# Kernel tuning notes

Measured on AMD Instinct MI355X. Metric: run time of the kernel, lower is better.

The kernel has to match this reference:

```python
import jax, jax.numpy as jnp
import numpy as np

B, C, F, D = 128, 16, 128, 512


def setup_inputs() -> dict:
    key = jax.random.key(0)
    k1, k2 = jax.random.split(key)
    return {
        "c_feats": jax.random.normal(k1, (B, C, D), dtype=jnp.float32),
        "f_feats": jax.random.normal(k2, (B, F, D), dtype=jnp.float32),
    }


def _dtw_path_masks(S):
    """S: [P, c, f] per-pair similarity. Returns [P, c, f] 0/1 max-path masks.

    DP: D[i,j] = max(D[i-1,j], D[i,j-1], D[i-1,j-1]) + S[i-1,j-1], D[0,0]=0,
    borders -inf. Tie-break priority (up, left, diag) matches Python max().
    Row recurrence is vectorized: D[i,j] = Csum[j] + cummax_k<=j(A[k]-Csum[k-1])
    where A[k]=max(D[i-1,k], D[i-1,k-1]) (wavefront-free row-parallel form).
    """
    P_, c, f = S.shape
    NEG = -jnp.inf

    init = jnp.concatenate([jnp.zeros((P_, 1), S.dtype),
                            jnp.full((P_, f), NEG, S.dtype)], axis=1)  # D[0, 0..f]

    def row_step(prev, dt_row):
        # prev: [P, f+1] = D[i-1, 0..f]; dt_row: [P, f] = S[i-1, :]
        A = jnp.maximum(prev[:, 1:], prev[:, :-1])                  # max(D[i-1,j], D[i-1,j-1])
        Ccum = jnp.cumsum(dt_row, axis=1)
        Cm1 = jnp.concatenate([jnp.zeros((P_, 1), dt_row.dtype), Ccum[:, :-1]], axis=1)
        row = Ccum + jax.lax.cummax(A - Cm1, axis=1)                # D[i, 1..f]
        new_prev = jnp.concatenate([jnp.full((P_, 1), NEG, dt_row.dtype), row], axis=1)
        return new_prev, new_prev

    _, rows = jax.lax.scan(row_step, init, jnp.moveaxis(S, 1, 0))   # [c, P, f+1]
    Dm = jnp.moveaxis(jnp.concatenate([init[None], rows], axis=0), 1, 0)  # [P, c+1, f+1]

    # Predecessor choice per cell; argmax picks first max -> priority up,left,diag
    up = Dm[:, :-1, 1:]
    left = Dm[:, 1:, :-1]
    diag = Dm[:, :-1, :-1]
    mv = jnp.argmax(jnp.stack([up, left, diag], axis=-1), axis=-1).astype(jnp.int32)
    mv = jnp.pad(mv, ((0, 0), (1, 0), (1, 0)))                      # [P, c+1, f+1]

    pidx = jnp.arange(P_)

    def bt_step(carry, _):
        mask, i, j = carry
        active = (i > 0) | (j > 0)
        mask = mask.at[pidx, i - 1, j - 1].add(jnp.where(active, 1.0, 0.0).astype(mask.dtype))
        m = mv[pidx, i, j]
        di = jnp.where(m == 1, 0, 1)   # left keeps i
        dj = jnp.where(m == 0, 0, 1)   # up keeps j
        i = jnp.where(active, i - di, i)
        j = jnp.where(active, j - dj, j)
        return (mask, i, j), None

    mask0 = jnp.zeros((P_, c, f), jnp.float32)
    i0 = jnp.full((P_,), c, jnp.int32)
    j0 = jnp.full((P_,), f, jnp.int32)
    (mask, _, _), _ = jax.lax.scan(bt_step, (mask0, i0, j0), None, length=c + f)
    return mask


def reference(c_feats, f_feats):
    b, c, d = c_feats.shape
    f = f_feats.shape[1]
    xn = c_feats / jnp.linalg.norm(c_feats, axis=-1, keepdims=True)
    yn = f_feats / jnp.linalg.norm(f_feats, axis=-1, keepdims=True)
    # Source quirk: y row j is normalized only once outer index i reaches it
    # (y[i-1] bug), so S[i,j] uses normalized y[j] iff j <= i, raw y[j] otherwise.
    Sn = jnp.einsum('mcd,nfd->mncf', xn, yn)
    Sr = jnp.einsum('mcd,nfd->mncf', xn, f_feats)
    tri = jnp.arange(f)[None, :] <= jnp.arange(c)[:, None]          # [c, f]: j <= i
    S = jnp.where(tri, Sn, Sr).reshape(b * b, c, f)
    return _dtw_path_masks(S).reshape(b, b, c, f)
```

## Files before the change

kernel.cpp:

```cpp
#include <hip/hip_runtime.h>
#include <stdint.h>

#define M_TOT 2048
#define N_TOT 16384
#define K_TOT 512

typedef _Float16 f16x8 __attribute__((ext_vector_type(8)));
typedef float f32x4 __attribute__((ext_vector_type(4)));

#define AS1 __attribute__((address_space(1)))
#define AS3 __attribute__((address_space(3)))

__device__ __forceinline__ void ld_lds16(const void* g, void* l) {
    __builtin_amdgcn_global_load_lds((const AS1 void*)g, (AS3 void*)l, 16, 0, 0);
}

__device__ __forceinline__ void split4(float x0, float x1, float x2, float x3,
                                       uint2* hs, uint2* ls) {
    union U { _Float16 h[4]; uint2 u; } H, L;
    _Float16 h0 = (_Float16)x0; H.h[0] = h0; L.h[0] = (_Float16)(x0 - (float)h0);
    _Float16 h1 = (_Float16)x1; H.h[1] = h1; L.h[1] = (_Float16)(x1 - (float)h1);
    _Float16 h2 = (_Float16)x2; H.h[2] = h2; L.h[2] = (_Float16)(x2 - (float)h2);
    _Float16 h3 = (_Float16)x3; H.h[3] = h3; L.h[3] = (_Float16)(x3 - (float)h3);
    *hs = H.u; *ls = L.u;
}

__global__ __launch_bounds__(256) void norm_split_kernel(
    const float* __restrict__ c_feats, const float* __restrict__ f_feats,
    _Float16* __restrict__ Ah, _Float16* __restrict__ Al,
    _Float16* __restrict__ Bh, _Float16* __restrict__ Bl,
    float* __restrict__ normf)
{
    int wave = blockIdx.x * 4 + (threadIdx.x >> 6);
    int lane = threadIdx.x & 63;
    if (wave < 2048) {
        const float* row = c_feats + (size_t)wave * K_TOT;
        float4 v0 = ((const float4*)row)[lane];
        float4 v1 = ((const float4*)row)[lane + 64];
        double ss = (double)v0.x * v0.x + (double)v0.y * v0.y +
                    (double)v0.z * v0.z + (double)v0.w * v0.w +
                    (double)v1.x * v1.x + (double)v1.y * v1.y +
                    (double)v1.z * v1.z + (double)v1.w * v1.w;
        #pragma unroll
        for (int off = 32; off; off >>= 1) ss += __shfl_down(ss, off);
        double tot = __shfl(ss, 0);
        float nrm = sqrtf((float)tot);
        float a0 = v0.x / nrm, a1 = v0.y / nrm, a2 = v0.z / nrm, a3 = v0.w / nrm;
        float b0 = v1.x / nrm, b1 = v1.y / nrm, b2 = v1.z / nrm, b3 = v1.w / nrm;
        uint2 h, l;
        split4(a0, a1, a2, a3, &h, &l);
        ((uint2*)(Ah + (size_t)wave * K_TOT))[lane] = h;
        ((uint2*)(Al + (size_t)wave * K_TOT))[lane] = l;
        split4(b0, b1, b2, b3, &h, &l);
        ((uint2*)(Ah + (size_t)wave * K_TOT))[lane + 64] = h;
        ((uint2*)(Al + (size_t)wave * K_TOT))[lane + 64] = l;
    } else if (wave < 18432) {
        int fr = wave - 2048;
        const float* row = f_feats + (size_t)fr * K_TOT;
        float4 v0 = ((const float4*)row)[lane];
        float4 v1 = ((const float4*)row)[lane + 64];
        double ss = (double)v0.x * v0.x + (double)v0.y * v0.y +
                    (double)v0.z * v0.z + (double)v0.w * v0.w +
                    (double)v1.x * v1.x + (double)v1.y * v1.y +
                    (double)v1.z * v1.z + (double)v1.w * v1.w;
        #pragma unroll
        for (int off = 32; off; off >>= 1) ss += __shfl_down(ss, off);
        if (lane == 0) normf[fr] = sqrtf((float)ss);
        uint2 h, l;
        split4(v0.x, v0.y, v0.z, v0.w, &h, &l);
        ((uint2*)(Bh + (size_t)fr * K_TOT))[lane] = h;
        ((uint2*)(Bl + (size_t)fr * K_TOT))[lane] = l;
        split4(v1.x, v1.y, v1.z, v1.w, &h, &l);
        ((uint2*)(Bh + (size_t)fr * K_TOT))[lane + 64] = h;
        ((uint2*)(Bl + (size_t)fr * K_TOT))[lane + 64] = l;
    }
}

__global__ __launch_bounds__(256, 2) void mfma_gemm_kernel(
    const _Float16* __restrict__ Ah, const _Float16* __restrict__ Al,
    const _Float16* __restrict__ Bh, const _Float16* __restrict__ Bl,
    const float* __restrict__ normf,
    float* __restrict__ out)
{
    __shared__ _Float16 sAh[128 * 32];
    __shared__ _Float16 sAl[128 * 32];
    __shared__ _Float16 sBh[128 * 32];
    __shared__ _Float16 sBl[128 * 32];

    const int t = threadIdx.x;
    const int w = t >> 6, lane = t & 63;
    const int gm0 = blockIdx.y * 128, gn0 = blockIdx.x * 128;
    const int wm = (w & 1) * 64, wn = (w >> 1) * 64;
    const int fr = lane & 15, fq = lane >> 4;

    f32x4 acc[4][4] = {};

    const int l0 = w * 128 + lane;

    for (int k0 = 0; k0 < K_TOT; k0 += 32) {
        #pragma unroll
        for (int c = 0; c < 2; ++c) {
            int l = l0 + c * 64;
            int row = l >> 2, kq = l & 3;
            size_t goffA = (size_t)(gm0 + row) * K_TOT + k0 + kq * 8;
            size_t goffB = (size_t)(gn0 + row) * K_TOT + k0 + kq * 8;
            ld_lds16(Ah + goffA, sAh + (size_t)l * 8);
            ld_lds16(Al + goffA, sAl + (size_t)l * 8);
            ld_lds16(Bh + goffB, sBh + (size_t)l * 8);
            ld_lds16(Bl + goffB, sBl + (size_t)l * 8);
        }
        __syncthreads();

        f16x8 fah[4], fal[4], fbh[4], fbl[4];
        #pragma unroll
        for (int x = 0; x < 4; ++x) {
            int ar = (wm + x * 16 + fr) * 32 + fq * 8;
            int br = (wn + x * 16 + fr) * 32 + fq * 8;
            fah[x] = *(const f16x8*)(sAh + ar);
            fal[x] = *(const f16x8*)(sAl + ar);
            fbh[x] = *(const f16x8*)(sBh + br);
            fbl[x] = *(const f16x8*)(sBl + br);
        }
        #pragma unroll
        for (int mi = 0; mi < 4; ++mi)
            #pragma unroll
            for (int ni = 0; ni < 4; ++ni) {
                acc[mi][ni] = __builtin_amdgcn_mfma_f32_16x16x32_f16(fah[mi], fbl[ni], acc[mi][ni], 0, 0, 0);
                acc[mi][ni] = __builtin_amdgcn_mfma_f32_16x16x32_f16(fal[mi], fbh[ni], acc[mi][ni], 0, 0, 0);
                acc[mi][ni] = __builtin_amdgcn_mfma_f32_16x16x32_f16(fah[mi], fbh[ni], acc[mi][ni], 0, 0, 0);
            }
        __syncthreads();
    }

    const int nn = blockIdx.x;
    #pragma unroll
    for (int ni = 0; ni < 4; ++ni) {
        int col = wn + ni * 16 + fr;
        bool cn = (col < 16);
        float nf = 1.f;
        if (cn) nf = normf[gn0 + col];
        #pragma unroll
        for (int mi = 0; mi < 4; ++mi) {
            #pragma unroll
            for (int r = 0; r < 4; ++r) {
                int gm = gm0 + wm + mi * 16 + fq * 4 + r;
                int mm = gm >> 4, ii = gm & 15;
                float v = acc[mi][ni][r];
                if (cn && col <= ii) v /= nf;
                out[(((size_t)mm * 128 + nn) * 16 + ii) * 128 + col] = v;
            }
        }
    }
}

__global__ __launch_bounds__(256) void dtw_kernel(float* __restrict__ buf)
{
    __shared__ uint8_t mv_lds[4][4][2064];
    __shared__ int bounds[4][4][16];

    const int lane = threadIdx.x & 63;
    const int w = threadIdx.x >> 6;
    const int q = lane >> 4, r = lane & 15;
    const int pbase = blockIdx.x * 16 + w * 4;
    const int p = pbase + q;
    float* tile = buf + (size_t)p * 2048;
    const float4* row4 = (const float4*)(tile + r * 128);
    uint8_t* mymv = &mv_lds[w][q][0];

    const double NEG = -1e300;
    double Dp = NEG, Dp2 = NEG;
    float4 cur4 = {0, 0, 0, 0};
    float4 nxt4 = row4[0];

    for (int t = 0; t < 143; ++t) {
        int j = t - r;
        bool act = (j >= 0) & (j < 128);
        if (act & ((j & 3) == 0)) {
            cur4 = nxt4;
            if (j + 4 < 128) nxt4 = row4[(j >> 2) + 1];
        }
        int e = j & 3;
        float sv = (e == 0) ? cur4.x : (e == 1) ? cur4.y : (e == 2) ? cur4.z : cur4.w;
        double up = __shfl_up(Dp, 1);
        double dg = __shfl_up(Dp2, 1);
        double lf = Dp;
        if (r == 0) up = NEG;
        if (j == 0) {
            lf = NEG;
            dg = (r == 0) ? 0.0 : NEG;
        } else if (r == 0) {
            dg = NEG;
        }
        int m = (up >= lf && up >= dg) ? 0 : ((lf >= dg) ? 1 : 2);
        double Dc = fmax(up, fmax(lf, dg)) + (double)sv;
        if (act) mymv[j * 16 + r] = (uint8_t)m;
        Dp2 = Dp;
        Dp = Dc;
    }
    __syncthreads();

    if (r == 0) {
        int i = 16, jj = 128, hic = 127;
        for (int it = 0; it < 160; ++it) {
            if (i <= 0) break;
            int m = mymv[(jj - 1) * 16 + (i - 1)];
            if (m == 1) { --jj; continue; }
            bounds[w][q][i - 1] = (jj - 1) | (hic << 8);
            if (m == 2) --jj;
            --i;
            hic = jj - 1;
        }
    }
    __syncthreads();

    #pragma unroll 4
    for (int it = 0; it < 32; ++it) {
        int flat = it * 64 + lane;
        int q2 = flat >> 9;
        int rem = flat & 511;
        int ii = rem >> 5;
        int c4 = rem & 31;
        int b = bounds[w][q2][ii];
        int lo = b & 0xff, hi = (b >> 8) & 0xff;
        int j0 = c4 * 4;
        float4 v;
        v.x = (j0 + 0 >= lo && j0 + 0 <= hi) ? 1.f : 0.f;
        v.y = (j0 + 1 >= lo && j0 + 1 <= hi) ? 1.f : 0.f;
        v.z = (j0 + 2 >= lo && j0 + 2 <= hi) ? 1.f : 0.f;
        v.w = (j0 + 3 >= lo && j0 + 3 <= hi) ? 1.f : 0.f;
        float* tb = buf + (size_t)(pbase + q2) * 2048;
        *(float4*)(tb + ii * 128 + j0) = v;
    }
}

extern "C" void kernel_launch(void* const* d_in, const int* in_sizes, int n_in,
                              void* d_out, int out_size, void* d_ws, size_t ws_size,
                              hipStream_t stream)
{
    const float* c_feats = (const float*)d_in[0];
    const float* f_feats = (const float*)d_in[1];
    float* out = (float*)d_out;

    _Float16* Ah = (_Float16*)d_ws;
    _Float16* Al = Ah + (size_t)M_TOT * K_TOT;
    _Float16* Bh = Al + (size_t)M_TOT * K_TOT;
    _Float16* Bl = Bh + (size_t)N_TOT * K_TOT;
    float* normf = (float*)(Bl + (size_t)N_TOT * K_TOT);

    norm_split_kernel<<<4608, 256, 0, stream>>>(c_feats, f_feats, Ah, Al, Bh, Bl, normf);
    dim3 g(N_TOT / 128, M_TOT / 128);
    mfma_gemm_kernel<<<g, 256, 0, stream>>>(Ah, Al, Bh, Bl, normf, out);
    dtw_kernel<<<1024, 256, 0, stream>>>(out);
}
```

Baseline: 361.0 us.

## Fuse DTW path computation into GEMM epilogue via shared-memory similarity tiles

The GEMM kernel now stages each 64x128 half of its accumulator tile in shared memory, runs the wavefront DTW recurrence and backtrack per pair inside the same block, and writes the 0/1 masks directly. This removes the global write and re-read of the full similarity matrix and one kernel launch. In exchange, DTW runs with only one 16-lane group per wave active out of four (the other lanes compute redundantly), and the GEMM block is held longer, which may lower overlap and occupancy.

```diff
diff --git a/kernel.cpp b/kernel.cpp
--- a/kernel.cpp
+++ b/kernel.cpp
@@ -76,16 +76,27 @@
     }
 }
 
-__global__ __launch_bounds__(256, 2) void mfma_gemm_kernel(
+#define SST 136
+#define S_BYTES (4 * 16 * SST * 4)
+#define MV_OFF S_BYTES
+#define MV_STRIDE 2080
+#define BND_OFF (MV_OFF + 4 * MV_STRIDE)
+#define SMEM_BYTES (BND_OFF + 4 * 16 * 4)
+
+__global__ __launch_bounds__(256, 2) void fused_gemm_dtw_kernel(
     const _Float16* __restrict__ Ah, const _Float16* __restrict__ Al,
     const _Float16* __restrict__ Bh, const _Float16* __restrict__ Bl,
     const float* __restrict__ normf,
     float* __restrict__ out)
 {
-    __shared__ _Float16 sAh[128 * 32];
-    __shared__ _Float16 sAl[128 * 32];
-    __shared__ _Float16 sBh[128 * 32];
-    __shared__ _Float16 sBl[128 * 32];
+    __shared__ __align__(16) uint8_t smem[SMEM_BYTES];
+    _Float16* sAh = (_Float16*)smem;
+    _Float16* sAl = sAh + 4096;
+    _Float16* sBh = sAl + 4096;
+    _Float16* sBl = sBh + 4096;
+    float* Sl = (float*)smem;
+    uint8_t* mvl = smem + MV_OFF;
+    int* bnd = (int*)(smem + BND_OFF);
 
     const int t = threadIdx.x;
     const int w = t >> 6, lane = t & 63;
@@ -94,7 +105,6 @@
     const int fr = lane & 15, fq = lane >> 4;
 
     f32x4 acc[4][4] = {};
-
     const int l0 = w * 128 + lane;
 
     for (int k0 = 0; k0 < K_TOT; k0 += 32) {
@@ -133,103 +143,85 @@
     }
 
     const int nn = blockIdx.x;
-    #pragma unroll
-    for (int ni = 0; ni < 4; ++ni) {
-        int col = wn + ni * 16 + fr;
-        bool cn = (col < 16);
-        float nf = 1.f;
-        if (cn) nf = normf[gn0 + col];
-        #pragma unroll
-        for (int mi = 0; mi < 4; ++mi) {
+    const double NEG = -1e300;
+
+    for (int b = 0; b < 2; ++b) {
+        __syncthreads();
+        if ((w & 1) == b) {
             #pragma unroll
-            for (int r = 0; r < 4; ++r) {
-                int gm = gm0 + wm + mi * 16 + fq * 4 + r;
-                int mm = gm >> 4, ii = gm & 15;
-                float v = acc[mi][ni][r];
-                if (cn && col <= ii) v /= nf;
-                out[(((size_t)mm * 128 + nn) * 16 + ii) * 128 + col] = v;
-            }
-        }
-    }
-}
-
-__global__ __launch_bounds__(256) void dtw_kernel(float* __restrict__ buf)
-{
-    __shared__ uint8_t mv_lds[4][4][2064];
-    __shared__ int bounds[4][4][16];
-
-    const int lane = threadIdx.x & 63;
-    const int w = threadIdx.x >> 6;
-    const int q = lane >> 4, r = lane & 15;
-    const int pbase = blockIdx.x * 16 + w * 4;
-    const int p = pbase + q;
-    float* tile = buf + (size_t)p * 2048;
-    const float4* row4 = (const float4*)(tile + r * 128);
-    uint8_t* mymv = &mv_lds[w][q][0];
-
-    const double NEG = -1e300;
-    double Dp = NEG, Dp2 = NEG;
-    float4 cur4 = {0, 0, 0, 0};
-    float4 nxt4 = row4[0];
-
-    for (int t = 0; t < 143; ++t) {
-        int j = t - r;
-        bool act = (j >= 0) & (j < 128);
-        if (act & ((j & 3) == 0)) {
-            cur4 = nxt4;
-            if (j + 4 < 128) nxt4 = row4[(j >> 2) + 1];
-        }
-        int e = j & 3;
-        float sv = (e == 0) ? cur4.x : (e == 1) ? cur4.y : (e == 2) ? cur4.z : cur4.w;
-        double up = __shfl_up(Dp, 1);
-        double dg = __shfl_up(Dp2, 1);
-        double lf = Dp;
-        if (r == 0) up = NEG;
-        if (j == 0) {
-            lf = NEG;
-            dg = (r == 0) ? 0.0 : NEG;
-        } else if (r == 0) {
-            dg = NEG;
-        }
-        int m = (up >= lf && up >= dg) ? 0 : ((lf >= dg) ? 1 : 2);
-        double Dc = fmax(up, fmax(lf, dg)) + (double)sv;
-        if (act) mymv[j * 16 + r] = (uint8_t)m;
-        Dp2 = Dp;
-        Dp = Dc;
-    }
-    __syncthreads();
-
-    if (r == 0) {
-        int i = 16, jj = 128, hic = 127;
-        for (int it = 0; it < 160; ++it) {
-            if (i <= 0) break;
-            int m = mymv[(jj - 1) * 16 + (i - 1)];
-            if (m == 1) { --jj; continue; }
-            bounds[w][q][i - 1] = (jj - 1) | (hic << 8);
-            if (m == 2) --jj;
-            --i;
-            hic = jj - 1;
-        }
-    }
-    __syncthreads();
-
-    #pragma unroll 4
-    for (int it = 0; it < 32; ++it) {
-        int flat = it * 64 + lane;
-        int q2 = flat >> 9;
-        int rem = flat & 511;
-        int ii = rem >> 5;
-        int c4 = rem & 31;
-        int b = bounds[w][q2][ii];
-        int lo = b & 0xff, hi = (b >> 8) & 0xff;
-        int j0 = c4 * 4;
-        float4 v;
-        v.x = (j0 + 0 >= lo && j0 + 0 <= hi) ? 1.f : 0.f;
-        v.y = (j0 + 1 >= lo && j0 + 1 <= hi) ? 1.f : 0.f;
-        v.z = (j0 + 2 >= lo && j0 + 2 <= hi) ? 1.f : 0.f;
-        v.w = (j0 + 3 >= lo && j0 + 3 <= hi) ? 1.f : 0.f;
-        float* tb = buf + (size_t)(pbase + q2) * 2048;
-        *(float4*)(tb + ii * 128 + j0) = v;
+            for (int ni = 0; ni < 4; ++ni) {
+                int col = wn + ni * 16 + fr;
+                bool cn = (col < 16);
+                float nf = cn ? normf[gn0 + col] : 1.f;
+                #pragma unroll
+                for (int mi = 0; mi < 4; ++mi) {
+                    #pragma unroll
+                    for (int rp = 0; rp < 4; ++rp) {
+                        int rr = fq * 4 + rp;
+                        float v = acc[mi][ni][rp];
+                        if (cn && col <= rr) v /= nf;
+                        Sl[(mi * 16 + rr) * SST + col] = v;
+                    }
+                }
+            }
+        }
+        __syncthreads();
+
+        const float* Srow = Sl + (w * 16 + fr) * SST;
+        uint8_t* mymv = mvl + w * MV_STRIDE;
+        double Dp = NEG, Dp2 = NEG;
+        for (int st = 0; st < 143; ++st) {
+            int j = st - fr;
+            bool act = (j >= 0) && (j < 128);
+            int jc = act ? j : 0;
+            float sv = Srow[jc];
+            double up = __shfl_up(Dp, 1);
+            double dg = __shfl_up(Dp2, 1);
+            double lf = Dp;
+            if (fr == 0) up = NEG;
+            if (j == 0) {
+                lf = NEG;
+                dg = (fr == 0) ? 0.0 : NEG;
+            } else if (fr == 0) {
+                dg = NEG;
+            }
+            int m = (up >= lf && up >= dg) ? 0 : ((lf >= dg) ? 1 : 2);
+            double Dc = fmax(up, fmax(lf, dg)) + (double)sv;
+            if (act && fq == 0) mymv[j * 16 + fr] = (uint8_t)m;
+            Dp2 = Dp;
+            Dp = Dc;
+        }
+        __syncthreads();
+
+        if (lane == 0) {
+            int i = 16, jj = 128, hic = 127;
+            for (int it = 0; it < 160; ++it) {
+                if (i <= 0) break;
+                int m = mymv[(jj - 1) * 16 + (i - 1)];
+                if (m == 1) { --jj; continue; }
+                bnd[w * 16 + i - 1] = (jj - 1) | (hic << 8);
+                if (m == 2) --jj;
+                --i;
+                hic = jj - 1;
+            }
+        }
+        __syncthreads();
+
+        float* tb = out + (size_t)((blockIdx.y * 8 + b * 4 + w) * 128 + nn) * 2048;
+        #pragma unroll
+        for (int it = 0; it < 8; ++it) {
+            int flat = it * 64 + lane;
+            int ii = flat >> 5, c4 = flat & 31;
+            int bb = bnd[w * 16 + ii];
+            int lo = bb & 0xff, hi = (bb >> 8) & 0xff;
+            int j0 = c4 * 4;
+            float4 v;
+            v.x = (j0 + 0 >= lo && j0 + 0 <= hi) ? 1.f : 0.f;
+            v.y = (j0 + 1 >= lo && j0 + 1 <= hi) ? 1.f : 0.f;
+            v.z = (j0 + 2 >= lo && j0 + 2 <= hi) ? 1.f : 0.f;
+            v.w = (j0 + 3 >= lo && j0 + 3 <= hi) ? 1.f : 0.f;
+            *(float4*)(tb + ii * 128 + j0) = v;
+        }
     }
 }
 
@@ -249,6 +241,5 @@
 
     norm_split_kernel<<<4608, 256, 0, stream>>>(c_feats, f_feats, Ah, Al, Bh, Bl, normf);
     dim3 g(N_TOT / 128, M_TOT / 128);
-    mfma_gemm_kernel<<<g, 256, 0, stream>>>(Ah, Al, Bh, Bl, normf, out);
-    dtw_kernel<<<1024, 256, 0, stream>>>(out);
-}
+    fused_gemm_dtw_kernel<<<g, 256, 0, stream>>>(Ah, Al, Bh, Bl, normf, out);
+}
```

After: 445.6 us. 1.23x slower.
